# Performance work log

Hardware: AMD Instinct MI355X
Metric: run time of the kernel (lower is better)

The kernel has to match this reference:

```python
import jax, jax.numpy as jnp
import numpy as np

B, T, C, H = 2, 2048, 1024, 16
HD = C // H            # 64
LAYER_IDX, N_LAYER = 5, 12
BASE = 16
# window_mode='power_2.0': progress=(5+1)/12=0.5; window=max(16, int(16+0.5**2*(2048-16)))=524
WINDOW = max(BASE, int(BASE + ((LAYER_IDX + 1) / N_LAYER) ** 2.0 * (T - BASE)))
WINDOW = min(WINDOW, T)


def setup_inputs() -> dict:
    key = jax.random.key(0)
    ks = jax.random.split(key, 6)
    x = jax.random.normal(ks[0], (B, T, C), dtype=jnp.float32)
    Wq = jax.random.normal(ks[1], (C, C), dtype=jnp.float32) * 0.02
    Wk = jax.random.normal(ks[2], (C, C), dtype=jnp.float32) * 0.02
    Wv = jax.random.normal(ks[3], (C, C), dtype=jnp.float32) * 0.02
    Wo = jax.random.normal(ks[4], (C, C), dtype=jnp.float32) * 0.02
    # RoPE tables: angles theta_i = t / 10000^(i/(HD/2)), shape (T,1,HD//2) to broadcast over (B,T,H,HD//2)
    half = HD // 2
    inv_freq = 1.0 / (10000.0 ** (jnp.arange(half, dtype=jnp.float32) / half))
    ang = jnp.arange(T, dtype=jnp.float32)[:, None] * inv_freq[None, :]  # (T, half)
    rope_cos = jnp.cos(ang)[:, None, :]  # (T,1,half)
    rope_sin = jnp.sin(ang)[:, None, :]
    return {"x": x, "Wq": Wq, "Wk": Wk, "Wv": Wv, "Wo": Wo,
            "rope_cos": rope_cos, "rope_sin": rope_sin}


def _apply_rotary(x, cos, sin):
    d = x.shape[-1] // 2
    x1, x2 = x[..., :d], x[..., d:]
    return jnp.concatenate([x1 * cos + x2 * sin, -x2 * sin + x1 * cos], axis=-1)


def reference(x, Wq, Wk, Wv, Wo, rope_cos, rope_sin):
    Bv, Tv, Cv = x.shape
    q = (x @ Wq).reshape(Bv, Tv, H, HD)
    k = (x @ Wk).reshape(Bv, Tv, H, HD)
    v = (x @ Wv).reshape(Bv, Tv, H, HD)
    q = _apply_rotary(q, rope_cos, rope_sin)
    k = _apply_rotary(k, rope_cos, rope_sin)
    # sliding-window causal mask: cols<=rows and cols>=rows-WINDOW+1
    rows = jnp.arange(Tv)[:, None]
    cols = jnp.arange(Tv)[None, :]
    allowed = (cols <= rows) & (cols >= rows - WINDOW + 1)  # (T,T)
    scale = 1.0 / np.sqrt(HD)
    scores = jnp.einsum('bthd,bshd->bhts', q, k) * scale  # (B,H,T,T)
    scores = jnp.where(allowed[None, None], scores, -jnp.inf)
    attn = jax.nn.softmax(scores, axis=-1)
    y = jnp.einsum('bhts,bshd->bthd', attn, v).reshape(Bv, Tv, Cv)
    return y @ Wo
```

## Files before the change

### kernel.cpp

```cpp
#include <hip/hip_runtime.h>
#include <math.h>

typedef unsigned short u16;
typedef unsigned int u32;
typedef __bf16 bf16x8 __attribute__((ext_vector_type(8)));
typedef float f32x4 __attribute__((ext_vector_type(4)));
typedef unsigned short ushort4v __attribute__((ext_vector_type(4)));

#define T_SEQ 2048
#define WIN_M1 523
#define QSCALE 0.180336879f
#define MASKV -1e30f

__device__ __forceinline__ u16 f2b(float f) {
  union { float f; unsigned int u; } v; v.f = f;
  unsigned int u = v.u;
  u += 0x7FFFu + ((u >> 16) & 1u);
  return (u16)(u >> 16);
}

__device__ __forceinline__ u32 cvtpk(float lo, float hi) {
  union { __bf16 h[2]; u32 d; } cv;
  cv.h[0] = (__bf16)lo;
  cv.h[1] = (__bf16)hi;
  return cv.d;
}

__device__ __forceinline__ float fexp2(float x) {
  return __builtin_amdgcn_exp2f(x);
}

__device__ __forceinline__ void load_lds16(const u16* g, u16* l) {
  __builtin_amdgcn_global_load_lds(
      (const __attribute__((address_space(1))) void*)g,
      (__attribute__((address_space(3))) void*)l, 16, 0, 0);
}


__global__ void prep_k(const float* __restrict__ x, u16* __restrict__ xb,
                       const float* __restrict__ W0, const float* __restrict__ W1,
                       const float* __restrict__ W2, const float* __restrict__ W3,
                       u16* __restrict__ WcatT, u16* __restrict__ WoT) {
  const int bid = blockIdx.x;
  if (bid < 4096) {
    int i = bid * 256 + threadIdx.x;
    float4 v = ((const float4*)x)[i];
    u16* d = xb + i * 4;
    d[0] = f2b(v.x); d[1] = f2b(v.y); d[2] = f2b(v.z); d[3] = f2b(v.w);
    return;
  }
  __shared__ float tile[32][33];
  const int t = bid - 4096;
  const int z = t >> 10, i = t & 1023;
  const float* W = (z == 0) ? W0 : (z == 1) ? W1 : (z == 2) ? W2 : W3;
  u16* Wt = (z < 3) ? (WcatT + (size_t)z * 1024 * 1024) : WoT;
  int tx = threadIdx.x & 31, ty = threadIdx.x >> 5;
  int n0 = (i & 31) * 32, k0 = (i >> 5) * 32;
#pragma unroll
  for (int j = 0; j < 4; ++j)
    tile[ty + j * 8][tx] = W[(size_t)(k0 + ty + j * 8) * 1024 + n0 + tx];
  __syncthreads();
#pragma unroll
  for (int j = 0; j < 4; ++j)
    Wt[(size_t)(n0 + ty + j * 8) * 1024 + k0 + tx] = f2b(tile[tx][ty + j * 8]);
}

template <int MODE>
__global__ __launch_bounds__(512, 6) void gemm_k(
    const u16* __restrict__ A, const u16* __restrict__ Bt,
    float* __restrict__ outf,
    u16* __restrict__ Qo, u16* __restrict__ Ko, u16* __restrict__ Vto,
    const float* __restrict__ rc, const float* __restrict__ rs) {
  __shared__ alignas(16) u16 As[3][128 * 32];
  __shared__ alignas(16) u16 Bs[3][128 * 32];
  const int tid = threadIdx.x, lane = tid & 63, w = tid >> 6;
  const int l15 = lane & 15, q4 = lane >> 4;
  const int row0 = blockIdx.y * 128, col0 = blockIdx.x * 128;
  const int wm = w >> 1, wn = w & 1;
  constexpr int NT = 32;

  f32x4 acc[2][4];
#pragma unroll
  for (int i = 0; i < 2; ++i)
#pragma unroll
    for (int j = 0; j < 4; ++j) acc[i][j] = (f32x4){0.f, 0.f, 0.f, 0.f};

  const int rs_ = w * 16 + (lane >> 2), cs_ = (lane & 3) * 8;
  const u16* gA0 = A + (size_t)(row0 + rs_) * 1024 + cs_;
  const u16* gB0 = Bt + (size_t)(col0 + rs_) * 1024 + cs_;
  const int soff = w * 512;

  auto stage = [&](int buf, int t) {
    const int k0 = t * 32;
    load_lds16(gA0 + k0, &As[buf][soff]);
    load_lds16(gB0 + k0, &Bs[buf][soff]);
  };
  auto compute = [&](int buf) {
    bf16x8 af[2], bfr[4];
#pragma unroll
    for (int im = 0; im < 2; ++im)
      af[im] = *(const bf16x8*)&As[buf][(wm * 32 + im * 16 + l15) * 32 + q4 * 8];
#pragma unroll
    for (int jn = 0; jn < 4; ++jn)
      bfr[jn] = *(const bf16x8*)&Bs[buf][(wn * 64 + jn * 16 + l15) * 32 + q4 * 8];
#pragma unroll
    for (int im = 0; im < 2; ++im)
#pragma unroll
      for (int jn = 0; jn < 4; ++jn)
        acc[im][jn] = __builtin_amdgcn_mfma_f32_16x16x32_bf16(af[im], bfr[jn], acc[im][jn], 0, 0, 0);
  };

  stage(0, 0);
  stage(1, 1);
  int bs = 2, bc = 0;
  for (int t = 0; t + 2 < NT; ++t) {
    stage(bs, t + 2);
    asm volatile("s_waitcnt vmcnt(4)" ::: "memory");
    __builtin_amdgcn_s_barrier();
    compute(bc);
    __builtin_amdgcn_s_barrier();
    bs = (bs + 1 == 3) ? 0 : bs + 1;
    bc = (bc + 1 == 3) ? 0 : bc + 1;
  }
  asm volatile("s_waitcnt vmcnt(2)" ::: "memory");
  __builtin_amdgcn_s_barrier();
  compute(bc);
  __builtin_amdgcn_s_barrier();
  bc = (bc + 1 == 3) ? 0 : bc + 1;
  asm volatile("s_waitcnt vmcnt(0)" ::: "memory");
  __builtin_amdgcn_s_barrier();
  compute(bc);

  if constexpr (MODE == 0) {
#pragma unroll
    for (int im = 0; im < 2; ++im) {
      const int rowb = row0 + wm * 32 + im * 16 + q4 * 4;
      const int b = rowb >> 11, t0 = rowb & 2047;
#pragma unroll
      for (int jn = 0; jn < 2; ++jn) {
        const int n = col0 + wn * 64 + jn * 16 + l15;
        const int sel = n >> 10, nn = n & 1023;
        const int h = nn >> 6, hd = nn & 63;
        const int bhi = b * 16 + h;
        if (sel < 2) {
          const float qs = (sel == 0) ? QSCALE : 1.0f;
          u16* base = (sel == 0 ? Qo : Ko);
          const int q4c = (hd >> 3) & 3, e = hd & 7;
#pragma unroll
          for (int r = 0; r < 4; ++r) {
            const int tt = t0 + r;
            const float c = rc[tt * 32 + hd], s = rs[tt * 32 + hd];
            const float x1 = acc[im][jn][r], x2 = acc[im][jn + 2][r];
            const size_t blk = ((size_t)bhi * 128 + (tt >> 4)) * 2;
            const size_t off = (size_t)q4c * 128 + (size_t)(tt & 15) * 8 + e;
            base[(blk << 9) + off] = f2b((x1 * c + x2 * s) * qs);
            base[((blk + 1) << 9) + off] = f2b((x1 * c - x2 * s) * qs);
          }
        } else {
          const int kv32 = t0 >> 5;
          const int q4w = (t0 >> 3) & 3;
          const int e0 = t0 & 7;
          const int jo1 = hd >> 4;
          const int l15r = hd & 15;
          ushort4v p1, p2;
#pragma unroll
          for (int r = 0; r < 4; ++r) {
            p1[r] = f2b(acc[im][jn][r]);
            p2[r] = f2b(acc[im][jn + 2][r]);
          }
          const size_t off = (size_t)q4w * 128 + (size_t)l15r * 8 + e0;
          const size_t b1 = ((((size_t)bhi * 64 + kv32) * 4 + jo1) << 9) + off;
          const size_t b2 = ((((size_t)bhi * 64 + kv32) * 4 + jo1 + 2) << 9) + off;
          *(ushort4v*)(Vto + b1) = p1;
          *(ushort4v*)(Vto + b2) = p2;
        }
      }
    }
  } else {
#pragma unroll
    for (int im = 0; im < 2; ++im) {
      const int rowb = row0 + wm * 32 + im * 16 + q4 * 4;
#pragma unroll
      for (int jn = 0; jn < 4; ++jn) {
        const int n = col0 + wn * 64 + jn * 16 + l15;
#pragma unroll
        for (int r = 0; r < 4; ++r)
          outf[(size_t)(rowb + r) * 1024 + n] = acc[im][jn][r];
      }
    }
  }
}

__global__ __launch_bounds__(256) void attn_k(
    const u16* __restrict__ Q, const u16* __restrict__ Kk,
    const u16* __restrict__ Vt, u16* __restrict__ Y) {
  const int lane = threadIdx.x & 63, w = threadIdx.x >> 6;
  const int l15 = lane & 15, q4 = lane >> 4;
  const int hw = blockIdx.x;
  const int work = (hw & 7) * 64 + (hw >> 3);
  const int bh = work >> 4;
  const int qt = 15 - (work & 15);
  const int q0 = qt * 128 + w * 32;
  const int qt16 = q0 >> 4;

  bf16x8 bq[2][2];
#pragma unroll
  for (int qs = 0; qs < 2; ++qs)
#pragma unroll
    for (int kb = 0; kb < 2; ++kb)
      bq[qs][kb] = *(const bf16x8*)(Q + ((((size_t)bh * 128 + qt16 + qs) * 2 + kb) << 9) + lane * 8);

  f32x4 o[2][4];
#pragma unroll
  for (int qs = 0; qs < 2; ++qs)
#pragma unroll
    for (int jo = 0; jo < 4; ++jo) o[qs][jo] = (f32x4){0.f, 0.f, 0.f, 0.f};
  float lp[2] = {0.f, 0.f};

  int s0 = q0 - WIN_M1; if (s0 < 0) s0 = 0; s0 &= ~31;
  const int srcA = l15 + ((q4 & 1) << 5);
  const int srcB = srcA + 16;
  const bool lowq4 = (q4 < 2);

  bf16x8 kc[2][2], kn[2][2];
  bf16x8 vc[4], vn[4];
#pragma unroll
  for (int ks = 0; ks < 2; ++ks)
#pragma unroll
    for (int kb = 0; kb < 2; ++kb)
      kc[ks][kb] = *(const bf16x8*)(Kk + ((((size_t)bh * 128 + (s0 >> 4) + ks) * 2 + kb) << 9) + lane * 8);
#pragma unroll
  for (int jo = 0; jo < 4; ++jo)
    vc[jo] = *(const bf16x8*)(Vt + ((((size_t)bh * 64 + (s0 >> 5)) * 4 + jo) << 9) + lane * 8);

  int kv0 = s0;

#define TILE_BODY(KC, VC, KN, VN)                                                      \
  {                                                                                    \
    const int kvn = kv0 + 32;                                                          \
    if (kvn <= q0) {                                                                   \
      _Pragma("unroll") for (int ks = 0; ks < 2; ++ks)                                 \
          _Pragma("unroll") for (int kb = 0; kb < 2; ++kb)                             \
              KN[ks][kb] = *(const bf16x8*)(Kk +                                       \
                  ((((size_t)bh * 128 + (kvn >> 4) + ks) * 2 + kb) << 9) + lane * 8);  \
      _Pragma("unroll") for (int jo = 0; jo < 4; ++jo)                                 \
          VN[jo] = *(const bf16x8*)(Vt +                                               \
              ((((size_t)bh * 64 + (kvn >> 5)) * 4 + jo) << 9) + lane * 8);            \
    }                                                                                  \
    f32x4 ss[2][2];                                                                    \
    _Pragma("unroll") for (int ks = 0; ks < 2; ++ks)                                   \
        _Pragma("unroll") for (int qs = 0; qs < 2; ++qs)                               \
            ss[ks][qs] = (f32x4){0.f, 0.f, 0.f, 0.f};                                  \
    _Pragma("unroll") for (int kb = 0; kb < 2; ++kb)                                   \
        _Pragma("unroll") for (int ks = 0; ks < 2; ++ks)                               \
            _Pragma("unroll") for (int qs = 0; qs < 2; ++qs)                           \
                ss[ks][qs] = __builtin_amdgcn_mfma_f32_16x16x32_bf16(                  \
                    KC[ks][kb], bq[qs][kb], ss[ks][qs], 0, 0, 0);                      \
    if ((kv0 + 32 > q0) || (kv0 < q0 - 492)) {                                         \
      _Pragma("unroll") for (int qs = 0; qs < 2; ++qs) {                               \
        const int tq = q0 + qs * 16 + l15;                                             \
        _Pragma("unroll") for (int ks = 0; ks < 2; ++ks)                               \
            _Pragma("unroll") for (int r = 0; r < 4; ++r) {                            \
          const int kv = kv0 + ks * 16 + q4 * 4 + r;                                   \
          if (kv > tq || kv < tq - WIN_M1) ss[ks][qs][r] = MASKV;                      \
        }                                                                              \
      }                                                                                \
    }                                                                                  \
    _Pragma("unroll") for (int qs = 0; qs < 2; ++qs) {                                 \
      float p[2][4];                                                                   \
      _Pragma("unroll") for (int ks = 0; ks < 2; ++ks)                                 \
          _Pragma("unroll") for (int r = 0; r < 4; ++r)                                \
              p[ks][r] = fexp2(ss[ks][qs][r]);                                         \
      lp[qs] += ((p[0][0] + p[0][1]) + (p[0][2] + p[0][3])) +                          \
                ((p[1][0] + p[1][1]) + (p[1][2] + p[1][3]));                           \
      const u32 a0 = cvtpk(p[0][0], p[0][1]), a1 = cvtpk(p[0][2], p[0][3]);            \
      const u32 b0 = cvtpk(p[1][0], p[1][1]), b1 = cvtpk(p[1][2], p[1][3]);            \
      union { u32 d[4]; bf16x8 v; } pu;                                                \
      const u32 d0a = (u32)__shfl((int)a0, srcA), d0b = (u32)__shfl((int)b0, srcA);    \
      const u32 d1a = (u32)__shfl((int)a1, srcA), d1b = (u32)__shfl((int)b1, srcA);    \
      const u32 d2a = (u32)__shfl((int)a0, srcB), d2b = (u32)__shfl((int)b0, srcB);    \
      const u32 d3a = (u32)__shfl((int)a1, srcB), d3b = (u32)__shfl((int)b1, srcB);    \
      pu.d[0] = lowq4 ? d0a : d0b;                                                     \
      pu.d[1] = lowq4 ? d1a : d1b;                                                     \
      pu.d[2] = lowq4 ? d2a : d2b;                                                     \
      pu.d[3] = lowq4 ? d3a : d3b;                                                     \
      _Pragma("unroll") for (int jo = 0; jo < 4; ++jo)                                 \
          o[qs][jo] = __builtin_amdgcn_mfma_f32_16x16x32_bf16(pu.v, VC[jo],            \
                                                              o[qs][jo], 0, 0, 0);     \
    }                                                                                  \
  }

  while (true) {
    TILE_BODY(kc, vc, kn, vn);
    kv0 += 32; if (kv0 > q0) break;
    TILE_BODY(kn, vn, kc, vc);
    kv0 += 32; if (kv0 > q0) break;
  }
#undef TILE_BODY

  const int b = bh >> 4, h = bh & 15;
  u16* Yb = Y + (size_t)(b * 2048 + q0) * 1024 + h * 64 + l15;
#pragma unroll
  for (int qs = 0; qs < 2; ++qs) {
    float l = lp[qs];
    l += __shfl_xor(l, 16);
    l += __shfl_xor(l, 32);
#pragma unroll
    for (int r = 0; r < 4; ++r) {
      const float lv = __shfl(l, q4 * 4 + r);
      const float inv = 1.0f / lv;
      u16* yr = Yb + (size_t)(qs * 16 + q4 * 4 + r) * 1024;
#pragma unroll
      for (int jo = 0; jo < 4; ++jo) yr[jo * 16] = f2b(o[qs][jo][r] * inv);
    }
  }
}

extern "C" void kernel_launch(void* const* d_in, const int* in_sizes, int n_in,
                              void* d_out, int out_size, void* d_ws, size_t ws_size,
                              hipStream_t stream) {
  const float* x = (const float*)d_in[0];
  const float* Wq = (const float*)d_in[1];
  const float* Wk = (const float*)d_in[2];
  const float* Wv = (const float*)d_in[3];
  const float* Wo = (const float*)d_in[4];
  const float* rc = (const float*)d_in[5];
  const float* rs = (const float*)d_in[6];
  float* out = (float*)d_out;
  char* ws = (char*)d_ws;
  const size_t MB = 1024 * 1024;
  u16* xb = (u16*)(ws);
  u16* WcatT = (u16*)(ws + 8 * MB);
  u16* WoT = (u16*)(ws + 14 * MB);
  u16* Qf = (u16*)(ws + 16 * MB);
  u16* Kf = (u16*)(ws + 24 * MB);
  u16* Vf = (u16*)(ws + 32 * MB);
  u16* Y = (u16*)(ws + 40 * MB);

  prep_k<<<8192, 256, 0, stream>>>(x, xb, Wq, Wk, Wv, Wo, WcatT, WoT);
  gemm_k<0><<<dim3(24, 32), 512, 0, stream>>>(xb, WcatT, nullptr, Qf, Kf, Vf, rc, rs);
  attn_k<<<512, 256, 0, stream>>>(Qf, Kf, Vf, Y);
  gemm_k<1><<<dim3(8, 32), 512, 0, stream>>>(Y, WoT, out, nullptr, nullptr, nullptr, nullptr, nullptr);
}
```

Before: 107.9 us.

## Store GEMM operands in MFMA fragment layout and load directly without LDS

The prep kernel now writes x and the weights in a pre-swizzled 16x32 MFMA fragment layout, and attention writes Y in that same layout. Both GEMMs can then load fragments straight from global memory into registers with register double-buffering, dropping the LDS staging and barriers. The QKV GEMM moves to 256 threads with a 64x64 tile per warp, and both GEMMs get XCD-aware block mapping, with the output GEMM using 128x64 tiles. The trade-off is no LDS sharing between warps, so each warp fetches its own operands from L2, which may raise cache traffic and memory latency exposure.

After: 105.2 us. -2.6%, faster.

```diff
diff --git a/kernel.cpp b/kernel.cpp
--- a/kernel.cpp
+++ b/kernel.cpp
@@ -30,30 +30,27 @@
   return __builtin_amdgcn_exp2f(x);
 }
 
-__device__ __forceinline__ void load_lds16(const u16* g, u16* l) {
-  __builtin_amdgcn_global_load_lds(
-      (const __attribute__((address_space(1))) void*)g,
-      (__attribute__((address_space(3))) void*)l, 16, 0, 0);
-}
-
-
-__global__ void prep_k(const float* __restrict__ x, u16* __restrict__ xb,
+
+__global__ void prep_k(const float* __restrict__ x, u16* __restrict__ xf,
                        const float* __restrict__ W0, const float* __restrict__ W1,
                        const float* __restrict__ W2, const float* __restrict__ W3,
-                       u16* __restrict__ WcatT, u16* __restrict__ WoT) {
+                       u16* __restrict__ WcatF, u16* __restrict__ WoF) {
   const int bid = blockIdx.x;
   if (bid < 4096) {
     int i = bid * 256 + threadIdx.x;
+    const int row = i >> 8, k = (i & 255) * 4;
     float4 v = ((const float4*)x)[i];
-    u16* d = xb + i * 4;
-    d[0] = f2b(v.x); d[1] = f2b(v.y); d[2] = f2b(v.z); d[3] = f2b(v.w);
+    ushort4v p = {f2b(v.x), f2b(v.y), f2b(v.z), f2b(v.w)};
+    const size_t blk = ((size_t)(row >> 4) * 32 + (k >> 5)) << 9;
+    const size_t off = (size_t)((k >> 3) & 3) * 128 + (size_t)(row & 15) * 8 + (k & 7);
+    *(ushort4v*)(xf + blk + off) = p;
     return;
   }
   __shared__ float tile[32][33];
   const int t = bid - 4096;
   const int z = t >> 10, i = t & 1023;
   const float* W = (z == 0) ? W0 : (z == 1) ? W1 : (z == 2) ? W2 : W3;
-  u16* Wt = (z < 3) ? (WcatT + (size_t)z * 1024 * 1024) : WoT;
+  u16* Wt = (z < 3) ? (WcatF + (size_t)z * 1024 * 1024) : WoF;
   int tx = threadIdx.x & 31, ty = threadIdx.x >> 5;
   int n0 = (i & 31) * 32, k0 = (i >> 5) * 32;
 #pragma unroll
@@ -61,23 +58,118 @@
     tile[ty + j * 8][tx] = W[(size_t)(k0 + ty + j * 8) * 1024 + n0 + tx];
   __syncthreads();
 #pragma unroll
-  for (int j = 0; j < 4; ++j)
-    Wt[(size_t)(n0 + ty + j * 8) * 1024 + k0 + tx] = f2b(tile[tx][ty + j * 8]);
-}
-
-template <int MODE>
-__global__ __launch_bounds__(512, 6) void gemm_k(
+  for (int j = 0; j < 4; ++j) {
+    const int n = n0 + ty + j * 8, k = k0 + tx;
+    const size_t blk = ((size_t)(n >> 4) * 32 + (k >> 5)) << 9;
+    const size_t off = (size_t)((k >> 3) & 3) * 128 + (size_t)(n & 15) * 8 + (k & 7);
+    Wt[blk + off] = f2b(tile[tx][ty + j * 8]);
+  }
+}
+
+__global__ __launch_bounds__(256) void gemm_qkv(
     const u16* __restrict__ A, const u16* __restrict__ Bt,
-    float* __restrict__ outf,
     u16* __restrict__ Qo, u16* __restrict__ Ko, u16* __restrict__ Vto,
     const float* __restrict__ rc, const float* __restrict__ rs) {
-  __shared__ alignas(16) u16 As[3][128 * 32];
-  __shared__ alignas(16) u16 Bs[3][128 * 32];
-  const int tid = threadIdx.x, lane = tid & 63, w = tid >> 6;
+  const int lane = threadIdx.x & 63, w = threadIdx.x >> 6;
   const int l15 = lane & 15, q4 = lane >> 4;
-  const int row0 = blockIdx.y * 128, col0 = blockIdx.x * 128;
+  const int g = blockIdx.x, xcd = g & 7, idx = g >> 3;
+  const int bx = xcd * 3 + idx % 3, by = idx / 3;
+  const int row0 = by * 128, col0 = bx * 128;
   const int wm = w >> 1, wn = w & 1;
-  constexpr int NT = 32;
+  const u16* Ab = A + (((size_t)((row0 >> 4) + wm * 4) * 32) << 9) + lane * 8;
+  const u16* Bb = Bt + (((size_t)((col0 >> 4) + wn * 4) * 32) << 9) + lane * 8;
+
+  f32x4 acc[4][4];
+#pragma unroll
+  for (int i = 0; i < 4; ++i)
+#pragma unroll
+    for (int j = 0; j < 4; ++j) acc[i][j] = (f32x4){0.f, 0.f, 0.f, 0.f};
+
+  bf16x8 ac[4], an[4], bc[4], bn[4];
+#pragma unroll
+  for (int im = 0; im < 4; ++im) ac[im] = *(const bf16x8*)(Ab + ((size_t)(im * 32) << 9));
+#pragma unroll
+  for (int jn = 0; jn < 4; ++jn) bc[jn] = *(const bf16x8*)(Bb + ((size_t)(jn * 32) << 9));
+
+  for (int t = 0; t < 32; t += 2) {
+#pragma unroll
+    for (int im = 0; im < 4; ++im) an[im] = *(const bf16x8*)(Ab + ((size_t)(im * 32 + t + 1) << 9));
+#pragma unroll
+    for (int jn = 0; jn < 4; ++jn) bn[jn] = *(const bf16x8*)(Bb + ((size_t)(jn * 32 + t + 1) << 9));
+#pragma unroll
+    for (int im = 0; im < 4; ++im)
+#pragma unroll
+      for (int jn = 0; jn < 4; ++jn)
+        acc[im][jn] = __builtin_amdgcn_mfma_f32_16x16x32_bf16(ac[im], bc[jn], acc[im][jn], 0, 0, 0);
+    if (t + 2 < 32) {
+#pragma unroll
+      for (int im = 0; im < 4; ++im) ac[im] = *(const bf16x8*)(Ab + ((size_t)(im * 32 + t + 2) << 9));
+#pragma unroll
+      for (int jn = 0; jn < 4; ++jn) bc[jn] = *(const bf16x8*)(Bb + ((size_t)(jn * 32 + t + 2) << 9));
+    }
+#pragma unroll
+    for (int im = 0; im < 4; ++im)
+#pragma unroll
+      for (int jn = 0; jn < 4; ++jn)
+        acc[im][jn] = __builtin_amdgcn_mfma_f32_16x16x32_bf16(an[im], bn[jn], acc[im][jn], 0, 0, 0);
+  }
+
+#pragma unroll
+  for (int im = 0; im < 4; ++im) {
+    const int rowb = row0 + wm * 64 + im * 16 + q4 * 4;
+    const int b = rowb >> 11, t0 = rowb & 2047;
+#pragma unroll
+    for (int jn = 0; jn < 2; ++jn) {
+      const int n = col0 + wn * 64 + jn * 16 + l15;
+      const int sel = n >> 10, nn = n & 1023;
+      const int h = nn >> 6, hd = nn & 63;
+      const int bhi = b * 16 + h;
+      if (sel < 2) {
+        const float qs = (sel == 0) ? QSCALE : 1.0f;
+        u16* base = (sel == 0 ? Qo : Ko);
+        const int q4c = (hd >> 3) & 3, e = hd & 7;
+#pragma unroll
+        for (int r = 0; r < 4; ++r) {
+          const int tt = t0 + r;
+          const float c = rc[tt * 32 + hd], s = rs[tt * 32 + hd];
+          const float x1 = acc[im][jn][r], x2 = acc[im][jn + 2][r];
+          const size_t blk = ((size_t)bhi * 128 + (tt >> 4)) * 2;
+          const size_t off = (size_t)q4c * 128 + (size_t)(tt & 15) * 8 + e;
+          base[(blk << 9) + off] = f2b((x1 * c + x2 * s) * qs);
+          base[((blk + 1) << 9) + off] = f2b((x1 * c - x2 * s) * qs);
+        }
+      } else {
+        const int kv32 = t0 >> 5;
+        const int q4w = (t0 >> 3) & 3;
+        const int e0 = t0 & 7;
+        const int jo1 = hd >> 4;
+        const int l15r = hd & 15;
+        ushort4v p1, p2;
+#pragma unroll
+        for (int r = 0; r < 4; ++r) {
+          p1[r] = f2b(acc[im][jn][r]);
+          p2[r] = f2b(acc[im][jn + 2][r]);
+        }
+        const size_t off = (size_t)q4w * 128 + (size_t)l15r * 8 + e0;
+        const size_t b1 = ((((size_t)bhi * 64 + kv32) * 4 + jo1) << 9) + off;
+        const size_t b2 = ((((size_t)bhi * 64 + kv32) * 4 + jo1 + 2) << 9) + off;
+        *(ushort4v*)(Vto + b1) = p1;
+        *(ushort4v*)(Vto + b2) = p2;
+      }
+    }
+  }
+}
+
+__global__ __launch_bounds__(256) void gemm_out(
+    const u16* __restrict__ A, const u16* __restrict__ Bt,
+    float* __restrict__ outf) {
+  const int lane = threadIdx.x & 63, w = threadIdx.x >> 6;
+  const int l15 = lane & 15, q4 = lane >> 4;
+  const int g = blockIdx.x, xcd = g & 7, idx = g >> 3;
+  const int bx = xcd * 2 + (idx & 1), by = idx >> 1;
+  const int row0 = by * 128, col0 = bx * 64;
+  const u16* Ab = A + (((size_t)((row0 >> 4) + w * 2) * 32) << 9) + lane * 8;
+  const u16* Bb = Bt + (((size_t)(col0 >> 4) * 32) << 9) + lane * 8;
 
   f32x4 acc[2][4];
 #pragma unroll
@@ -85,115 +177,51 @@
 #pragma unroll
     for (int j = 0; j < 4; ++j) acc[i][j] = (f32x4){0.f, 0.f, 0.f, 0.f};
 
-  const int rs_ = w * 16 + (lane >> 2), cs_ = (lane & 3) * 8;
-  const u16* gA0 = A + (size_t)(row0 + rs_) * 1024 + cs_;
-  const u16* gB0 = Bt + (size_t)(col0 + rs_) * 1024 + cs_;
-  const int soff = w * 512;
-
-  auto stage = [&](int buf, int t) {
-    const int k0 = t * 32;
-    load_lds16(gA0 + k0, &As[buf][soff]);
-    load_lds16(gB0 + k0, &Bs[buf][soff]);
-  };
-  auto compute = [&](int buf) {
-    bf16x8 af[2], bfr[4];
+  bf16x8 ac[2], an[2], bc[4], bn[4];
+#pragma unroll
+  for (int im = 0; im < 2; ++im) ac[im] = *(const bf16x8*)(Ab + ((size_t)(im * 32) << 9));
+#pragma unroll
+  for (int jn = 0; jn < 4; ++jn) bc[jn] = *(const bf16x8*)(Bb + ((size_t)(jn * 32) << 9));
+
+  for (int t = 0; t < 32; t += 2) {
+#pragma unroll
+    for (int im = 0; im < 2; ++im) an[im] = *(const bf16x8*)(Ab + ((size_t)(im * 32 + t + 1) << 9));
+#pragma unroll
+    for (int jn = 0; jn < 4; ++jn) bn[jn] = *(const bf16x8*)(Bb + ((size_t)(jn * 32 + t + 1) << 9));
 #pragma unroll
     for (int im = 0; im < 2; ++im)
-      af[im] = *(const bf16x8*)&As[buf][(wm * 32 + im * 16 + l15) * 32 + q4 * 8];
-#pragma unroll
-    for (int jn = 0; jn < 4; ++jn)
-      bfr[jn] = *(const bf16x8*)&Bs[buf][(wn * 64 + jn * 16 + l15) * 32 + q4 * 8];
+#pragma unroll
+      for (int jn = 0; jn < 4; ++jn)
+        acc[im][jn] = __builtin_amdgcn_mfma_f32_16x16x32_bf16(ac[im], bc[jn], acc[im][jn], 0, 0, 0);
+    if (t + 2 < 32) {
+#pragma unroll
+      for (int im = 0; im < 2; ++im) ac[im] = *(const bf16x8*)(Ab + ((size_t)(im * 32 + t + 2) << 9));
+#pragma unroll
+      for (int jn = 0; jn < 4; ++jn) bc[jn] = *(const bf16x8*)(Bb + ((size_t)(jn * 32 + t + 2) << 9));
+    }
 #pragma unroll
     for (int im = 0; im < 2; ++im)
 #pragma unroll
       for (int jn = 0; jn < 4; ++jn)
-        acc[im][jn] = __builtin_amdgcn_mfma_f32_16x16x32_bf16(af[im], bfr[jn], acc[im][jn], 0, 0, 0);
-  };
-
-  stage(0, 0);
-  stage(1, 1);
-  int bs = 2, bc = 0;
-  for (int t = 0; t + 2 < NT; ++t) {
-    stage(bs, t + 2);
-    asm volatile("s_waitcnt vmcnt(4)" ::: "memory");
-    __builtin_amdgcn_s_barrier();
-    compute(bc);
-    __builtin_amdgcn_s_barrier();
-    bs = (bs + 1 == 3) ? 0 : bs + 1;
-    bc = (bc + 1 == 3) ? 0 : bc + 1;
-  }
-  asm volatile("s_waitcnt vmcnt(2)" ::: "memory");
-  __builtin_amdgcn_s_barrier();
-  compute(bc);
-  __builtin_amdgcn_s_barrier();
-  bc = (bc + 1 == 3) ? 0 : bc + 1;
-  asm volatile("s_waitcnt vmcnt(0)" ::: "memory");
-  __builtin_amdgcn_s_barrier();
-  compute(bc);
-
-  if constexpr (MODE == 0) {
-#pragma unroll
-    for (int im = 0; im < 2; ++im) {
-      const int rowb = row0 + wm * 32 + im * 16 + q4 * 4;
-      const int b = rowb >> 11, t0 = rowb & 2047;
-#pragma unroll
-      for (int jn = 0; jn < 2; ++jn) {
-        const int n = col0 + wn * 64 + jn * 16 + l15;
-        const int sel = n >> 10, nn = n & 1023;
-        const int h = nn >> 6, hd = nn & 63;
-        const int bhi = b * 16 + h;
-        if (sel < 2) {
-          const float qs = (sel == 0) ? QSCALE : 1.0f;
-          u16* base = (sel == 0 ? Qo : Ko);
-          const int q4c = (hd >> 3) & 3, e = hd & 7;
-#pragma unroll
-          for (int r = 0; r < 4; ++r) {
-            const int tt = t0 + r;
-            const float c = rc[tt * 32 + hd], s = rs[tt * 32 + hd];
-            const float x1 = acc[im][jn][r], x2 = acc[im][jn + 2][r];
-            const size_t blk = ((size_t)bhi * 128 + (tt >> 4)) * 2;
-            const size_t off = (size_t)q4c * 128 + (size_t)(tt & 15) * 8 + e;
-            base[(blk << 9) + off] = f2b((x1 * c + x2 * s) * qs);
-            base[((blk + 1) << 9) + off] = f2b((x1 * c - x2 * s) * qs);
-          }
-        } else {
-          const int kv32 = t0 >> 5;
-          const int q4w = (t0 >> 3) & 3;
-          const int e0 = t0 & 7;
-          const int jo1 = hd >> 4;
-          const int l15r = hd & 15;
-          ushort4v p1, p2;
-#pragma unroll
-          for (int r = 0; r < 4; ++r) {
-            p1[r] = f2b(acc[im][jn][r]);
-            p2[r] = f2b(acc[im][jn + 2][r]);
-          }
-          const size_t off = (size_t)q4w * 128 + (size_t)l15r * 8 + e0;
-          const size_t b1 = ((((size_t)bhi * 64 + kv32) * 4 + jo1) << 9) + off;
-          const size_t b2 = ((((size_t)bhi * 64 + kv32) * 4 + jo1 + 2) << 9) + off;
-          *(ushort4v*)(Vto + b1) = p1;
-          *(ushort4v*)(Vto + b2) = p2;
-        }
-      }
-    }
-  } else {
-#pragma unroll
-    for (int im = 0; im < 2; ++im) {
-      const int rowb = row0 + wm * 32 + im * 16 + q4 * 4;
-#pragma unroll
-      for (int jn = 0; jn < 4; ++jn) {
-        const int n = col0 + wn * 64 + jn * 16 + l15;
-#pragma unroll
-        for (int r = 0; r < 4; ++r)
-          outf[(size_t)(rowb + r) * 1024 + n] = acc[im][jn][r];
-      }
+        acc[im][jn] = __builtin_amdgcn_mfma_f32_16x16x32_bf16(an[im], bn[jn], acc[im][jn], 0, 0, 0);
+  }
+
+#pragma unroll
+  for (int im = 0; im < 2; ++im) {
+    const int rowb = row0 + w * 32 + im * 16 + q4 * 4;
+#pragma unroll
+    for (int jn = 0; jn < 4; ++jn) {
+      const int n = col0 + jn * 16 + l15;
+#pragma unroll
+      for (int r = 0; r < 4; ++r)
+        outf[(size_t)(rowb + r) * 1024 + n] = acc[im][jn][r];
     }
   }
 }
 
 __global__ __launch_bounds__(256) void attn_k(
     const u16* __restrict__ Q, const u16* __restrict__ Kk,
-    const u16* __restrict__ Vt, u16* __restrict__ Y) {
+    const u16* __restrict__ Vt, u16* __restrict__ Yf) {
   const int lane = threadIdx.x & 63, w = threadIdx.x >> 6;
   const int l15 = lane & 15, q4 = lane >> 4;
   const int hw = blockIdx.x;
@@ -299,7 +327,7 @@
 #undef TILE_BODY
 
   const int b = bh >> 4, h = bh & 15;
-  u16* Yb = Y + (size_t)(b * 2048 + q0) * 1024 + h * 64 + l15;
+  const int r16base = (b * 2048 + q0) >> 4;
 #pragma unroll
   for (int qs = 0; qs < 2; ++qs) {
     float l = lp[qs];
@@ -309,9 +337,14 @@
     for (int r = 0; r < 4; ++r) {
       const float lv = __shfl(l, q4 * 4 + r);
       const float inv = 1.0f / lv;
-      u16* yr = Yb + (size_t)(qs * 16 + q4 * 4 + r) * 1024;
-#pragma unroll
-      for (int jo = 0; jo < 4; ++jo) yr[jo * 16] = f2b(o[qs][jo][r] * inv);
+#pragma unroll
+      for (int jo = 0; jo < 4; ++jo) {
+        const int k32 = h * 2 + (jo >> 1);
+        const int q4f = ((jo & 1) << 1) | (l15 >> 3);
+        const size_t blk = ((size_t)(r16base + qs) * 32 + k32) << 9;
+        const size_t off = (size_t)q4f * 128 + (size_t)(q4 * 4 + r) * 8 + (l15 & 7);
+        Yf[blk + off] = f2b(o[qs][jo][r] * inv);
+      }
     }
   }
 }
@@ -329,16 +362,16 @@
   float* out = (float*)d_out;
   char* ws = (char*)d_ws;
   const size_t MB = 1024 * 1024;
-  u16* xb = (u16*)(ws);
-  u16* WcatT = (u16*)(ws + 8 * MB);
-  u16* WoT = (u16*)(ws + 14 * MB);
+  u16* xf = (u16*)(ws);
+  u16* WcatF = (u16*)(ws + 8 * MB);
+  u16* WoF = (u16*)(ws + 14 * MB);
   u16* Qf = (u16*)(ws + 16 * MB);
   u16* Kf = (u16*)(ws + 24 * MB);
   u16* Vf = (u16*)(ws + 32 * MB);
-  u16* Y = (u16*)(ws + 40 * MB);
-
-  prep_k<<<8192, 256, 0, stream>>>(x, xb, Wq, Wk, Wv, Wo, WcatT, WoT);
-  gemm_k<0><<<dim3(24, 32), 512, 0, stream>>>(xb, WcatT, nullptr, Qf, Kf, Vf, rc, rs);
-  attn_k<<<512, 256, 0, stream>>>(Qf, Kf, Vf, Y);
-  gemm_k<1><<<dim3(8, 32), 512, 0, stream>>>(Y, WoT, out, nullptr, nullptr, nullptr, nullptr, nullptr);
-}
+  u16* Yf = (u16*)(ws + 40 * MB);
+
+  prep_k<<<8192, 256, 0, stream>>>(x, xf, Wq, Wk, Wv, Wo, WcatF, WoF);
+  gemm_qkv<<<768, 256, 0, stream>>>(xf, WcatF, Qf, Kf, Vf, rc, rs);
+  attn_k<<<512, 256, 0, stream>>>(Qf, Kf, Vf, Yf);
+  gemm_out<<<512, 256, 0, stream>>>(Yf, WoF, out);
+}
```
